# Kernel optimization log

Hardware: AMD Instinct MI355X
Metric: run time of the kernel (lower is better)

## Reference

```python
import jax, jax.numpy as jnp
import numpy as np

BETA = 0.25
ENTROPY_LOSS_RATIO = 0.1
TEMPERATURE = 0.01
EPS = 1e-5


def _l2norm(x):
    return x / jnp.sqrt(jnp.sum(x * x, axis=-1, keepdims=True)).clip(1e-12)


def _entropy_loss(affinity):
    # affinity: [N, n_e]
    a = affinity / TEMPERATURE
    probs = jax.nn.softmax(a, axis=-1)
    log_probs = jax.nn.log_softmax(a + EPS, axis=-1)
    avg_probs = jnp.mean(probs, axis=0)
    avg_entropy = -jnp.sum(avg_probs * jnp.log(avg_probs + EPS))
    sample_entropy = -jnp.mean(jnp.sum(probs * log_probs, axis=-1))
    return sample_entropy - avg_entropy


def setup_inputs() -> dict:
    key = jax.random.key(0)
    k1, k2, k3 = jax.random.split(key, 3)
    B, C, H, W = 16, 256, 32, 32
    n_e = 16384
    z = jax.random.normal(k1, (B, C, H, W), dtype=jnp.float32)
    embedding = jax.random.normal(k2, (n_e, C), dtype=jnp.float32) * 0.02
    query_ids = jax.random.randint(k3, (B, 1), 0, W, dtype=jnp.int64)
    return {"z": z, "embedding": embedding, "query_ids": query_ids}


def reference(z, embedding, query_ids):
    B, C, H, W = z.shape
    sg = jax.lax.stop_gradient
    zt = jnp.transpose(z, (0, 2, 3, 1))            # [B,H,W,C]
    # l2_norm=True path
    zt = _l2norm(zt)
    emb = _l2norm(embedding)                       # [n_e, C]
    zf = zt.reshape(-1, C)                         # [N, C]
    d = (jnp.sum(zf * zf, axis=1, keepdims=True)
         + jnp.sum(emb * emb, axis=1)
         - 2.0 * jnp.einsum('nd,kd->nk', zf, emb))  # [N, n_e]
    idx = jnp.argmin(d, axis=1)                    # [N]
    z_q = emb[idx].reshape(zt.shape)               # [B,H,W,C]

    # dead code rate (unbiased std over batch, per token position)
    code = idx.reshape(B, -1).astype(jnp.float32)
    dead_code_rate = jnp.mean((jnp.std(code, axis=0, ddof=1) < 1e-5).astype(jnp.float32))

    vq_loss = jnp.mean((z_q - sg(zt)) ** 2, axis=-1, keepdims=True)      # [B,H,W,1]
    commit_loss = BETA * jnp.mean((sg(z_q) - zt) ** 2, axis=-1, keepdims=True)
    loss_mask = (jnp.arange(W).reshape(1, 1, -1, 1)
                 <= query_ids[:, -1].reshape(-1, 1, 1, 1)).astype(jnp.float32)
    denom = jnp.sum(loss_mask)
    vq_loss = jnp.sum(vq_loss * loss_mask) / denom
    commit_loss = jnp.sum(commit_loss * loss_mask) / denom
    entropy_loss = ENTROPY_LOSS_RATIO * _entropy_loss(-d)

    # straight-through estimator
    z_q_st = zt + sg(z_q - zt)
    z_q_out = jnp.transpose(z_q_st, (0, 3, 1, 2))  # [B,C,H,W]
    return (z_q_out, vq_loss, commit_loss, entropy_loss, dead_code_rate, idx)
```

## Files before the change

kernel.cpp:

```cpp
#include <hip/hip_runtime.h>
#include <math.h>

#define N_TOK   16384
#define N_E     16384
#define CDIM    256
#define NCH     8
#define CHSZ    (N_E / NCH)
#define L2E100  144.26950408889634f
#define DELTA_C 0.06f
#define EPS_NT  0.008f
#define CAP_BLK 1536u
#define NT_CAP  65536u

typedef __attribute__((ext_vector_type(8))) short short8;
typedef __attribute__((ext_vector_type(4))) float f32x4;

#define OFF_A2   0u
#define OFF_B2   2097152u
#define OFF_RMX  4194304u
#define OFF_CS   4210688u
#define OFF_SC   4227072u
#define OFF_RK   4227088u
#define OFF_NT   4259856u
#define OFF_NTC  4325392u
#define OFF_CBC  4325408u
#define OFF_IDX  4327456u
#define OFF_CAND 4343840u
#define OFF_ZT   10635296u
#define NEED_ZT_BYTES 59318400ull

__device__ __forceinline__ unsigned short f2bf(float x) {
  unsigned u = __float_as_uint(x);
  unsigned r = (u + 0x7fffu + ((u >> 16) & 1u)) >> 16;
  return (unsigned short)r;
}
__device__ __forceinline__ float bf2f(unsigned short h) {
  return __uint_as_float(((unsigned)h) << 16);
}
__device__ __forceinline__ unsigned fkey(float f) {
  unsigned u = __float_as_uint(f);
  return (u & 0x80000000u) ? ~u : (u | 0x80000000u);
}
__device__ __forceinline__ float keyf(unsigned k) {
  return (k & 0x80000000u) ? __uint_as_float(k ^ 0x80000000u) : __uint_as_float(~k);
}

__device__ __forceinline__ void async_load16(const void* g, void* l) {
  __builtin_amdgcn_global_load_lds((const __attribute__((address_space(1))) void*)g,
                                   (__attribute__((address_space(3))) void*)l, 16, 0, 0);
}

__device__ __forceinline__ float blockReduceSum256(float v, float* sbuf) {
  __syncthreads();
  v += __shfl_down(v, 32);
  v += __shfl_down(v, 16);
  v += __shfl_down(v, 8);
  v += __shfl_down(v, 4);
  v += __shfl_down(v, 2);
  v += __shfl_down(v, 1);
  const int tid = threadIdx.x;
  if ((tid & 63) == 0) sbuf[tid >> 6] = v;
  __syncthreads();
  return sbuf[0] + sbuf[1] + sbuf[2] + sbuf[3];
}

__global__ __launch_bounds__(256) void k_norm_emb(const float* __restrict__ emb,
    unsigned short* __restrict__ B2, float* __restrict__ colsum,
    float* __restrict__ scalars, unsigned long long* __restrict__ rowkey,
    unsigned* __restrict__ ntc, unsigned* __restrict__ rowMaxU) {
  const int tid = threadIdx.x, lane = tid & 63, wv = tid >> 6;
  if (blockIdx.x < 64) {
    const int i = blockIdx.x * 256 + tid;
    colsum[i] = 0.f;
    rowkey[i] = ~0ull;
    rowMaxU[i] = 0u;
    if (i < 16) { scalars[i] = 0.f; ntc[i] = 0u; }
  }
  const int k = blockIdx.x * 4 + wv;
  const float4 v = *(const float4*)&emb[(size_t)k * CDIM + lane * 4];
  float ss = v.x * v.x + v.y * v.y + v.z * v.z + v.w * v.w;
#pragma unroll
  for (int off = 1; off < 64; off <<= 1) ss += __shfl_xor(ss, off);
  const float r = 1.0f / fmaxf(sqrtf(ss), 1e-12f);
  ushort4 o;
  o.x = f2bf(v.x * r); o.y = f2bf(v.y * r);
  o.z = f2bf(v.z * r); o.w = f2bf(v.w * r);
  *(ushort4*)&B2[(size_t)k * CDIM + lane * 4] = o;
}

__global__ __launch_bounds__(256) void k_norm_z(const float* __restrict__ z,
                                                unsigned short* __restrict__ A2,
                                                float* __restrict__ zT) {
  __shared__ float ssb[4][64];
  __shared__ float rn[64];
  __shared__ unsigned short tile[64 * 264];
  __shared__ float tileF[64 * 260];
  const int b = blockIdx.x >> 4, hw0 = (blockIdx.x & 15) * 64;
  const int tid = threadIdx.x, cg = tid >> 6, hwl = tid & 63;
  float ss = 0.f;
#pragma unroll 8
  for (int i = 0; i < 64; ++i) {
    const int c = cg + i * 4;
    const float x = z[((size_t)(b * CDIM + c) << 10) + hw0 + hwl];
    ss = fmaf(x, x, ss);
  }
  ssb[cg][hwl] = ss;
  __syncthreads();
  if (tid < 64) {
    const float t = ssb[0][tid] + ssb[1][tid] + ssb[2][tid] + ssb[3][tid];
    rn[tid] = 1.0f / fmaxf(sqrtf(t), 1e-12f);
  }
  __syncthreads();
  const float r = rn[hwl];
#pragma unroll 8
  for (int i = 0; i < 64; ++i) {
    const int c = cg + i * 4;
    const float x = z[((size_t)(b * CDIM + c) << 10) + hw0 + hwl];
    tile[hwl * 264 + c] = f2bf(x * r);
    tileF[hwl * 260 + c] = x;
  }
  __syncthreads();
  const int rr = tid >> 5, tt = tid & 31;
#pragma unroll
  for (int it = 0; it < 8; ++it) {
    const int row = rr + 8 * it;
    const int token = b * 1024 + hw0 + row;
    const uint4 v = *(const uint4*)&tile[row * 264 + tt * 8];
    *(uint4*)&A2[(size_t)token * CDIM + tt * 8] = v;
    if (zT != nullptr) {
      const float4 f0 = *(const float4*)&tileF[row * 260 + tt * 4];
      const float4 f1 = *(const float4*)&tileF[row * 260 + 128 + tt * 4];
      *(float4*)&zT[(size_t)token * CDIM + tt * 4] = f0;
      *(float4*)&zT[(size_t)token * CDIM + 128 + tt * 4] = f1;
    }
  }
}

__global__ __launch_bounds__(256, 3) void k_pass1(const unsigned short* __restrict__ A2,
    const unsigned short* __restrict__ B2,
    unsigned long long* __restrict__ cand, unsigned* __restrict__ cbc,
    unsigned* __restrict__ rowMaxU) {
  __shared__ alignas(16) unsigned short Bt[2][128 * 64];
  __shared__ unsigned smaxU[64];
  __shared__ unsigned lcnt;
  const int rt = blockIdx.x, chunk = blockIdx.y;
  const int r0 = rt * 64, k0 = chunk * CHSZ;
  const int blin = rt * NCH + chunk;
  const int tid = threadIdx.x, lane = tid & 63, w = tid >> 6;
  const int wrr = (w & 1) * 32, wc = (w >> 1) * 64;
  const int l15 = lane & 15, quad = lane >> 4;

  if (tid == 0) lcnt = 0u;
  if (tid < 64) smaxU[tid] = 0u;

  short8 afr[2][4][2];
#pragma unroll
  for (int ti = 0; ti < 2; ++ti) {
    const size_t rbase = (size_t)(r0 + wrr + ti * 16 + l15) * CDIM;
#pragma unroll
    for (int st = 0; st < 4; ++st)
#pragma unroll
      for (int kk = 0; kk < 2; ++kk)
        afr[ti][st][kk] = *(const short8*)&A2[rbase + st * 64 + (((kk << 2) | quad) * 8)];
  }

  const unsigned short* bsrc[4];
  unsigned bdst[4];
#pragma unroll
  for (int i = 0; i < 4; ++i) {
    const int lin = i * 256 + tid;
    const int row = lin >> 3, cg = lin & 7;
    const int gcg = cg ^ (row & 7);
    bsrc[i] = B2 + (size_t)(k0 + row) * CDIM + gcg * 8;
    bdst[i] = (unsigned)lin * 16u;
  }
#pragma unroll
  for (int i = 0; i < 4; ++i)
    async_load16(bsrc[i], (char*)Bt[0] + bdst[i]);

  int boff[4][2];
#pragma unroll
  for (int tj = 0; tj < 4; ++tj) {
    const int br = wc + tj * 16 + l15;
#pragma unroll
    for (int kk = 0; kk < 2; ++kk)
      boff[tj][kk] = br * 64 + ((((kk << 2) | quad) ^ (br & 7)) * 8);
  }
  __syncthreads();

  f32x4 acc[2][4];

  for (int ct = 0; ct < 16; ++ct) {
#pragma unroll
    for (int ti = 0; ti < 2; ++ti)
#pragma unroll
      for (int tj = 0; tj < 4; ++tj) acc[ti][tj] = (f32x4){0.f, 0.f, 0.f, 0.f};

#pragma unroll
    for (int st = 0; st < 4; ++st) {
      if (!(ct == 15 && st == 3)) {
        const int noff = (st < 3) ? (st + 1) * 64 : 32768;
        char* dbuf = (char*)Bt[(st + 1) & 1];
#pragma unroll
        for (int i = 0; i < 4; ++i)
          async_load16(bsrc[i] + noff, dbuf + bdst[i]);
      }
      const unsigned short* bp = Bt[st & 1];
#pragma unroll
      for (int kk = 0; kk < 2; ++kk) {
        short8 bfr[4];
#pragma unroll
        for (int tj = 0; tj < 4; ++tj)
          bfr[tj] = *(const short8*)&bp[boff[tj][kk]];
#pragma unroll
        for (int ti = 0; ti < 2; ++ti)
#pragma unroll
          for (int tj = 0; tj < 4; ++tj)
            acc[ti][tj] = __builtin_amdgcn_mfma_f32_16x16x32_bf16(afr[ti][st][kk], bfr[tj],
                                                                  acc[ti][tj], 0, 0, 0);
      }
      if (st == 3) {
        const int kb = k0 + ct * 128;
#pragma unroll
        for (int ti = 0; ti < 2; ++ti)
#pragma unroll
          for (int tj = 0; tj < 4; ++tj) {
            f32x4 a = acc[ti][tj];
#pragma unroll
            for (int r = 0; r < 4; ++r) a[r] = a[r] + a[r];
            acc[ti][tj] = a;
          }
#pragma unroll
        for (int ti = 0; ti < 2; ++ti)
#pragma unroll
          for (int r = 0; r < 4; ++r) {
            float mt = fmaxf(fmaxf(acc[ti][0][r], acc[ti][1][r]),
                             fmaxf(acc[ti][2][r], acc[ti][3][r]));
            mt = fmaxf(mt, __shfl_xor(mt, 1));
            mt = fmaxf(mt, __shfl_xor(mt, 2));
            mt = fmaxf(mt, __shfl_xor(mt, 4));
            mt = fmaxf(mt, __shfl_xor(mt, 8));
            if (l15 == 0) atomicMax(&smaxU[wrr + ti * 16 + quad * 4 + r], fkey(mt));
          }
        __syncthreads();
#pragma unroll
        for (int ti = 0; ti < 2; ++ti)
#pragma unroll
          for (int r = 0; r < 4; ++r) {
            const int rowloc = wrr + ti * 16 + quad * 4 + r;
            const float thr = keyf(smaxU[rowloc]) - DELTA_C;
            const unsigned rowg = (unsigned)(r0 + rowloc);
#pragma unroll
            for (int tj = 0; tj < 4; ++tj) {
              const float t = acc[ti][tj][r];
              if (t >= thr) {
                const unsigned slot = atomicAdd(&lcnt, 1u);
                if (slot < CAP_BLK) {
                  const unsigned pr = (rowg << 14) | (unsigned)(kb + wc + tj * 16 + l15);
                  cand[(size_t)blin * CAP_BLK + slot] =
                      ((unsigned long long)__float_as_uint(t) << 32) | pr;
                }
              }
            }
          }
      }
      __syncthreads();
    }
#pragma unroll
    for (int i = 0; i < 4; ++i) bsrc[i] += 32768;
  }
  if (tid < 64) atomicMax(&rowMaxU[r0 + tid], smaxU[tid]);
  if (tid == 0) cbc[blin] = lcnt < CAP_BLK ? lcnt : CAP_BLK;
}

__global__ __launch_bounds__(256) void k_cstat2(const unsigned long long* __restrict__ cand,
    const unsigned* __restrict__ cbc, const unsigned* __restrict__ rowMaxU,
    float* __restrict__ colsum, unsigned* __restrict__ ntList,
    unsigned* __restrict__ ntc, float* __restrict__ scalars) {
  __shared__ float lM[64], lZ[64], lE[64], lIZ[64];
  __shared__ float sbuf[4];
  const int rt = blockIdx.x, r0 = rt * 64;
  const int tid = threadIdx.x, lane = tid & 63;
  if (tid < 64) {
    lM[tid] = keyf(rowMaxU[r0 + tid]);
    lZ[tid] = 0.f; lE[tid] = 0.f;
  }
  __syncthreads();
  for (int sub = 0; sub < NCH; ++sub) {
    const int blin = rt * NCH + sub;
    const unsigned cnt = cbc[blin] < CAP_BLK ? cbc[blin] : CAP_BLK;
    for (unsigned i = tid; i < cnt; i += 256u) {
      const unsigned long long e = cand[(size_t)blin * CAP_BLK + i];
      const unsigned pr = (unsigned)(e & 0xFFFFFFFu);
      const float t = __uint_as_float((unsigned)(e >> 32));
      const int rowl = (int)((pr >> 14) & 63u);
      const float d = t - lM[rowl];
      const float ex = exp2f(d * L2E100);
      atomicAdd(&lZ[rowl], ex);
      atomicAdd(&lE[rowl], d * 100.0f * ex);
    }
  }
  __syncthreads();
  float ent = 0.f;
  if (tid < 64) {
    const float Z = lZ[tid];
    lIZ[tid] = 1.0f / Z;
    ent = logf(Z) - lE[tid] / Z;
  }
  const float es = blockReduceSum256(ent, sbuf);
  if (tid == 0) atomicAdd(&scalars[1], es);
  __syncthreads();
  for (int sub = 0; sub < NCH; ++sub) {
    const int blin = rt * NCH + sub;
    const unsigned cnt = cbc[blin] < CAP_BLK ? cbc[blin] : CAP_BLK;
    const unsigned lim = (cnt + 255u) & ~255u;
    for (unsigned i = tid; i < lim; i += 256u) {
      bool nt = false;
      unsigned pr = 0u;
      if (i < cnt) {
        const unsigned long long e = cand[(size_t)blin * CAP_BLK + i];
        pr = (unsigned)(e & 0xFFFFFFFu);
        const float t = __uint_as_float((unsigned)(e >> 32));
        const int rowl = (int)((pr >> 14) & 63u);
        const float d = t - lM[rowl];
        atomicAdd(&colsum[pr & 0x3FFFu], exp2f(d * L2E100) * lIZ[rowl]);
        nt = (d >= -EPS_NT);
      }
      const unsigned long long mask = __ballot(nt);
      const unsigned cw = (unsigned)__popcll(mask);
      unsigned base = 0u;
      if (lane == 0 && cw) base = atomicAdd(ntc, cw);
      base = __shfl((int)base, 0);
      if (nt) {
        const unsigned off = (unsigned)__popcll(mask & ((1ull << lane) - 1ull));
        const unsigned s = base + off;
        if (s < NT_CAP) ntList[s] = pr;
      }
    }
  }
}

__global__ __launch_bounds__(256) void k_refine(const float* __restrict__ z,
    const float* __restrict__ zT, const float* __restrict__ emb,
    const unsigned* __restrict__ ntList, const unsigned* __restrict__ ntc,
    unsigned long long* __restrict__ rowkey) {
  const unsigned cnt = *ntc;
  const unsigned lim = cnt < NT_CAP ? cnt : NT_CAP;
  const int lane = threadIdx.x & 63, wv = threadIdx.x >> 6;
  for (unsigned slot = blockIdx.x * 4 + wv; slot < lim; slot += gridDim.x * 4) {
    const unsigned pr = ntList[slot];
    const int n = (int)(pr >> 14), k = (int)(pr & 0x3FFFu);
    const int b = n >> 10, hw = n & 1023;
    double sz = 0.0, se = 0.0, sp = 0.0;
#pragma unroll
    for (int u = 0; u < CDIM / 64; ++u) {
      const int c = lane + u * 64;
      const double zv = (zT != nullptr)
          ? (double)zT[(size_t)n * CDIM + c]
          : (double)z[((size_t)(b * CDIM + c) << 10) + hw];
      const double ev = (double)emb[(size_t)k * CDIM + c];
      sz = fma(zv, zv, sz); se = fma(ev, ev, se); sp = fma(zv, ev, sp);
    }
    for (int off = 32; off; off >>= 1) {
      sz += __shfl_down(sz, off);
      se += __shfl_down(se, off);
      sp += __shfl_down(sp, off);
    }
    if (lane == 0) {
      const double nz = fmax(sqrt(sz), 1e-12);
      const double ne = fmax(sqrt(se), 1e-12);
      const double d = sz / (nz * nz) + se / (ne * ne) - 2.0 * sp / (nz * ne);
      const unsigned long long key =
          (((unsigned long long)(d * 140737488355328.0)) << 14) | (unsigned long long)k;
      atomicMin(&rowkey[n], key);
    }
  }
}

__global__ __launch_bounds__(256) void k_zq(const unsigned short* __restrict__ A2,
    const unsigned short* __restrict__ B2, const unsigned long long* __restrict__ rowkey,
    const long long* __restrict__ qids, int* __restrict__ idxI,
    float* __restrict__ outIdxF, float* __restrict__ outZ,
    float* __restrict__ scalars) {
  __shared__ int lidx[64];
  __shared__ unsigned short tile[64 * 264];
  __shared__ float sbuf[4];
  const int b = blockIdx.x >> 4, hw0 = (blockIdx.x & 15) * 64;
  const int tid = threadIdx.x;
  if (tid < 64) {
    const int n = b * 1024 + hw0 + tid;
    const unsigned long long key = rowkey[n];
    const int k = (key != ~0ull) ? (int)(key & 0x3FFFull) : 0;
    lidx[tid] = k;
    idxI[n] = k;
    outIdxF[n] = (float)k;
  }
  __syncthreads();
  const long long qid = qids[b];
  const int rr = tid >> 5, tt = tid & 31;
  float vq = 0.f;
#pragma unroll
  for (int it = 0; it < 8; ++it) {
    const int row = rr + 8 * it;
    const int token = b * 1024 + hw0 + row;
    union { uint4 v; unsigned short s[8]; } ev, zv;
    ev.v = *(const uint4*)&B2[(size_t)lidx[row] * CDIM + tt * 8];
    zv.v = *(const uint4*)&A2[(size_t)token * CDIM + tt * 8];
    *(uint4*)&tile[row * 264 + tt * 8] = ev.v;
    float dd = 0.f;
#pragma unroll
    for (int u = 0; u < 8; ++u) {
      const float d = bf2f(ev.s[u]) - bf2f(zv.s[u]);
      dd = fmaf(d, d, dd);
    }
    if ((long long)(row & 31) <= qid) vq += dd;
  }
  const float s = blockReduceSum256(vq, sbuf);
  if (tid == 0) atomicAdd(&scalars[0], s * (1.0f / 256.0f));
  __syncthreads();
  const int cg = tid >> 6, hwl = tid & 63;
#pragma unroll 8
  for (int i = 0; i < 64; ++i) {
    const int c = cg + i * 4;
    outZ[((size_t)(b * CDIM + c) << 10) + hw0 + hwl] = bf2f(tile[hwl * 264 + c]);
  }
}

__global__ __launch_bounds__(256) void k_final(const int* __restrict__ idxI,
    const long long* __restrict__ qids, const float* __restrict__ colsum,
    const float* __restrict__ scalars, float* __restrict__ out) {
  __shared__ float sbuf[4];
  const int tid = threadIdx.x;
  float ae = 0.f;
  for (int i = tid; i < N_E; i += 256) {
    const float q = colsum[i] * (1.0f / (float)N_TOK);
    ae += q * logf(q + 1e-5f);
  }
  const float aes = blockReduceSum256(ae, sbuf);
  int cnt = 0;
  for (int p = tid; p < 1024; p += 256) {
    const int v = idxI[p];
    bool eq = true;
    for (int b = 1; b < 16; ++b) eq = eq && (idxI[b * 1024 + p] == v);
    cnt += eq ? 1 : 0;
  }
  const float dc = blockReduceSum256((float)cnt, sbuf);
  if (tid == 0) {
    float denom = 0.f;
    for (int b = 0; b < 16; ++b) denom += (float)(qids[b] + 1ll);
    out[4194304] = scalars[0] / denom;
    out[4194305] = 0.25f * scalars[0] / denom;
    out[4194306] = 0.1f * (scalars[1] * (1.0f / (float)N_TOK) + aes);
    out[4194307] = dc * (1.0f / 1024.0f);
  }
}

extern "C" void kernel_launch(void* const* d_in, const int* in_sizes, int n_in,
                              void* d_out, int out_size, void* d_ws, size_t ws_size,
                              hipStream_t stream) {
  const float*      z    = (const float*)d_in[0];
  const float*      emb  = (const float*)d_in[1];
  const long long*  qids = (const long long*)d_in[2];
  float* out = (float*)d_out;
  float* W   = (float*)d_ws;

  unsigned short* A2 = (unsigned short*)(W + OFF_A2);
  unsigned short* B2 = (unsigned short*)(W + OFF_B2);
  unsigned* rowMaxU = (unsigned*)(W + OFF_RMX);
  float* colsum = W + OFF_CS;
  float* scal   = W + OFF_SC;
  unsigned long long* rowkey = (unsigned long long*)(W + OFF_RK);
  unsigned* ntList = (unsigned*)(W + OFF_NT);
  unsigned* ntc    = (unsigned*)(W + OFF_NTC);
  unsigned* cbc    = (unsigned*)(W + OFF_CBC);
  int* idxI        = (int*)(W + OFF_IDX);
  unsigned long long* cand = (unsigned long long*)(W + OFF_CAND);
  float* zT = (ws_size >= NEED_ZT_BYTES) ? (W + OFF_ZT) : (float*)nullptr;

  k_norm_emb<<<dim3(N_E / 4),     dim3(256), 0, stream>>>(emb, B2, colsum, scal,
                                                          rowkey, ntc, rowMaxU);
  k_norm_z  <<<dim3(256),         dim3(256), 0, stream>>>(z, A2, zT);
  k_pass1   <<<dim3(256, NCH),    dim3(256), 0, stream>>>(A2, B2, cand, cbc, rowMaxU);
  k_cstat2  <<<dim3(256),         dim3(256), 0, stream>>>(cand, cbc, rowMaxU, colsum,
                                                          ntList, ntc, scal);
  k_refine  <<<dim3(1024),        dim3(256), 0, stream>>>(z, zT, emb, ntList, ntc, rowkey);
  k_zq      <<<dim3(256),         dim3(256), 0, stream>>>(A2, B2, rowkey, qids,
                                                          idxI, out + 4194308, out, scal);
  k_final   <<<dim3(1),           dim3(256), 0, stream>>>(idxI, qids, colsum, scal, out);
}
```

Baseline: 641.3 us.

## Software-pipeline candidate epilogue behind next tile's MFMA with ping-pong accumulators

The GEMM-plus-candidate kernel now keeps two accumulator sets and runs the max-reduction and candidate-emit epilogue for the previous column tile while the MFMAs for the next tile are issued. The epilogue is split across the st==0 and st==1 stages, which also removes one extra __syncthreads per tile. MFMA sections are bracketed with s_setprio, and the per-lane B-load pointer arrays are replaced by a single base pointer plus constant offsets to save registers. In exchange, the doubled accumulators raise VGPR pressure, which could lower occupancy, and the last tile needs a duplicated epilogue after the loop.

```diff
diff --git a/kernel.cpp b/kernel.cpp
--- a/kernel.cpp
+++ b/kernel.cpp
@@ -164,19 +164,14 @@
         afr[ti][st][kk] = *(const short8*)&A2[rbase + st * 64 + (((kk << 2) | quad) * 8)];
   }
 
-  const unsigned short* bsrc[4];
-  unsigned bdst[4];
-#pragma unroll
-  for (int i = 0; i < 4; ++i) {
-    const int lin = i * 256 + tid;
-    const int row = lin >> 3, cg = lin & 7;
-    const int gcg = cg ^ (row & 7);
-    bsrc[i] = B2 + (size_t)(k0 + row) * CDIM + gcg * 8;
-    bdst[i] = (unsigned)lin * 16u;
-  }
+  const int row0 = tid >> 3, cg0 = tid & 7;
+  const int gcg0 = cg0 ^ (row0 & 7);
+  const unsigned short* bsrc0 = B2 + (size_t)(k0 + row0) * CDIM + gcg0 * 8;
+  const unsigned bofs0 = (unsigned)tid * 16u;
+
 #pragma unroll
   for (int i = 0; i < 4; ++i)
-    async_load16(bsrc[i], (char*)Bt[0] + bdst[i]);
+    async_load16(bsrc0 + i * 8192, (char*)Bt[0] + bofs0 + i * 4096);
 
   int boff[4][2];
 #pragma unroll
@@ -188,24 +183,28 @@
   }
   __syncthreads();
 
-  f32x4 acc[2][4];
-
-  for (int ct = 0; ct < 16; ++ct) {
+  f32x4 accA[2][4], accB[2][4];
+  size_t cbase = 0;
+
+  auto computeCt = [&](f32x4 (&aN)[2][4], f32x4 (&aO)[2][4], int ctNew, int doEpi) {
+    const int kbOld = k0 + (ctNew - 1) * 128;
+    const unsigned short* bs = bsrc0 + cbase;
 #pragma unroll
     for (int ti = 0; ti < 2; ++ti)
 #pragma unroll
-      for (int tj = 0; tj < 4; ++tj) acc[ti][tj] = (f32x4){0.f, 0.f, 0.f, 0.f};
+      for (int tj = 0; tj < 4; ++tj) aN[ti][tj] = (f32x4){0.f, 0.f, 0.f, 0.f};
 
 #pragma unroll
     for (int st = 0; st < 4; ++st) {
-      if (!(ct == 15 && st == 3)) {
+      if (!(ctNew == 15 && st == 3)) {
         const int noff = (st < 3) ? (st + 1) * 64 : 32768;
         char* dbuf = (char*)Bt[(st + 1) & 1];
 #pragma unroll
         for (int i = 0; i < 4; ++i)
-          async_load16(bsrc[i] + noff, dbuf + bdst[i]);
+          async_load16(bs + i * 8192 + noff, dbuf + bofs0 + i * 4096);
       }
       const unsigned short* bp = Bt[st & 1];
+      __builtin_amdgcn_s_setprio(1);
 #pragma unroll
       for (int kk = 0; kk < 2; ++kk) {
         short8 bfr[4];
@@ -216,33 +215,35 @@
         for (int ti = 0; ti < 2; ++ti)
 #pragma unroll
           for (int tj = 0; tj < 4; ++tj)
-            acc[ti][tj] = __builtin_amdgcn_mfma_f32_16x16x32_bf16(afr[ti][st][kk], bfr[tj],
-                                                                  acc[ti][tj], 0, 0, 0);
-      }
-      if (st == 3) {
-        const int kb = k0 + ct * 128;
+            aN[ti][tj] = __builtin_amdgcn_mfma_f32_16x16x32_bf16(afr[ti][st][kk], bfr[tj],
+                                                                 aN[ti][tj], 0, 0, 0);
+      }
+      __builtin_amdgcn_s_setprio(0);
+
+      if (doEpi && st == 0) {
 #pragma unroll
         for (int ti = 0; ti < 2; ++ti)
 #pragma unroll
           for (int tj = 0; tj < 4; ++tj) {
-            f32x4 a = acc[ti][tj];
+            f32x4 a = aO[ti][tj];
 #pragma unroll
             for (int r = 0; r < 4; ++r) a[r] = a[r] + a[r];
-            acc[ti][tj] = a;
+            aO[ti][tj] = a;
           }
 #pragma unroll
         for (int ti = 0; ti < 2; ++ti)
 #pragma unroll
           for (int r = 0; r < 4; ++r) {
-            float mt = fmaxf(fmaxf(acc[ti][0][r], acc[ti][1][r]),
-                             fmaxf(acc[ti][2][r], acc[ti][3][r]));
+            float mt = fmaxf(fmaxf(aO[ti][0][r], aO[ti][1][r]),
+                             fmaxf(aO[ti][2][r], aO[ti][3][r]));
             mt = fmaxf(mt, __shfl_xor(mt, 1));
             mt = fmaxf(mt, __shfl_xor(mt, 2));
             mt = fmaxf(mt, __shfl_xor(mt, 4));
             mt = fmaxf(mt, __shfl_xor(mt, 8));
             if (l15 == 0) atomicMax(&smaxU[wrr + ti * 16 + quad * 4 + r], fkey(mt));
           }
-        __syncthreads();
+      }
+      if (doEpi && st == 1) {
 #pragma unroll
         for (int ti = 0; ti < 2; ++ti)
 #pragma unroll
@@ -252,11 +253,11 @@
             const unsigned rowg = (unsigned)(r0 + rowloc);
 #pragma unroll
             for (int tj = 0; tj < 4; ++tj) {
-              const float t = acc[ti][tj][r];
+              const float t = aO[ti][tj][r];
               if (t >= thr) {
                 const unsigned slot = atomicAdd(&lcnt, 1u);
                 if (slot < CAP_BLK) {
-                  const unsigned pr = (rowg << 14) | (unsigned)(kb + wc + tj * 16 + l15);
+                  const unsigned pr = (rowg << 14) | (unsigned)(kbOld + wc + tj * 16 + l15);
                   cand[(size_t)blin * CAP_BLK + slot] =
                       ((unsigned long long)__float_as_uint(t) << 32) | pr;
                 }
@@ -266,9 +267,63 @@
       }
       __syncthreads();
     }
-#pragma unroll
-    for (int i = 0; i < 4; ++i) bsrc[i] += 32768;
-  }
+    cbase += 32768;
+  };
+
+  computeCt(accA, accB, 0, 0);
+#pragma unroll 1
+  for (int ctp = 0; ctp < 7; ++ctp) {
+    computeCt(accB, accA, 2 * ctp + 1, 1);
+    computeCt(accA, accB, 2 * ctp + 2, 1);
+  }
+  computeCt(accB, accA, 15, 1);
+
+  {
+    const int kb = k0 + 15 * 128;
+#pragma unroll
+    for (int ti = 0; ti < 2; ++ti)
+#pragma unroll
+      for (int tj = 0; tj < 4; ++tj) {
+        f32x4 a = accB[ti][tj];
+#pragma unroll
+        for (int r = 0; r < 4; ++r) a[r] = a[r] + a[r];
+        accB[ti][tj] = a;
+      }
+#pragma unroll
+    for (int ti = 0; ti < 2; ++ti)
+#pragma unroll
+      for (int r = 0; r < 4; ++r) {
+        float mt = fmaxf(fmaxf(accB[ti][0][r], accB[ti][1][r]),
+                         fmaxf(accB[ti][2][r], accB[ti][3][r]));
+        mt = fmaxf(mt, __shfl_xor(mt, 1));
+        mt = fmaxf(mt, __shfl_xor(mt, 2));
+        mt = fmaxf(mt, __shfl_xor(mt, 4));
+        mt = fmaxf(mt, __shfl_xor(mt, 8));
+        if (l15 == 0) atomicMax(&smaxU[wrr + ti * 16 + quad * 4 + r], fkey(mt));
+      }
+    __syncthreads();
+#pragma unroll
+    for (int ti = 0; ti < 2; ++ti)
+#pragma unroll
+      for (int r = 0; r < 4; ++r) {
+        const int rowloc = wrr + ti * 16 + quad * 4 + r;
+        const float thr = keyf(smaxU[rowloc]) - DELTA_C;
+        const unsigned rowg = (unsigned)(r0 + rowloc);
+#pragma unroll
+        for (int tj = 0; tj < 4; ++tj) {
+          const float t = accB[ti][tj][r];
+          if (t >= thr) {
+            const unsigned slot = atomicAdd(&lcnt, 1u);
+            if (slot < CAP_BLK) {
+              const unsigned pr = (rowg << 14) | (unsigned)(kb + wc + tj * 16 + l15);
+              cand[(size_t)blin * CAP_BLK + slot] =
+                  ((unsigned long long)__float_as_uint(t) << 32) | pr;
+            }
+          }
+        }
+      }
+  }
+  __syncthreads();
   if (tid < 64) atomicMax(&rowMaxU[r0 + tid], smaxU[tid]);
   if (tid == 0) cbc[blin] = lcnt < CAP_BLK ? lcnt : CAP_BLK;
 }
```

After: 960.1 us. 1.5x slower.

## Triple-buffer B tiles in pass1 with fine-grained vmcnt waits and priority hints

Applied to the files above, without the earlier changes.

The distance GEMM kernel moves from double to triple buffering of the codebook tile in LDS, so loads run two stages ahead. Full __syncthreads are replaced with explicit s_waitcnt vmcnt(4) plus raw s_barrier, letting one stage's loads stay in flight across the barrier. It also raises wave priority around the MFMA block. This hides global-load latency but uses more LDS per block, which may reduce occupancy, and relies on the hand-written waitcnt counts being correct.

```diff
diff --git a/kernel.cpp b/kernel.cpp
--- a/kernel.cpp
+++ b/kernel.cpp
@@ -140,7 +140,7 @@
     const unsigned short* __restrict__ B2,
     unsigned long long* __restrict__ cand, unsigned* __restrict__ cbc,
     unsigned* __restrict__ rowMaxU) {
-  __shared__ alignas(16) unsigned short Bt[2][128 * 64];
+  __shared__ alignas(16) unsigned short Bt[3][128 * 64];
   __shared__ unsigned smaxU[64];
   __shared__ unsigned lcnt;
   const int rt = blockIdx.x, chunk = blockIdx.y;
@@ -164,19 +164,10 @@
         afr[ti][st][kk] = *(const short8*)&A2[rbase + st * 64 + (((kk << 2) | quad) * 8)];
   }
 
-  const unsigned short* bsrc[4];
-  unsigned bdst[4];
-#pragma unroll
-  for (int i = 0; i < 4; ++i) {
-    const int lin = i * 256 + tid;
-    const int row = lin >> 3, cg = lin & 7;
-    const int gcg = cg ^ (row & 7);
-    bsrc[i] = B2 + (size_t)(k0 + row) * CDIM + gcg * 8;
-    bdst[i] = (unsigned)lin * 16u;
-  }
-#pragma unroll
-  for (int i = 0; i < 4; ++i)
-    async_load16(bsrc[i], (char*)Bt[0] + bdst[i]);
+  const int row0 = tid >> 3, cg0 = tid & 7;
+  const int gcg0 = cg0 ^ (row0 & 7);
+  const unsigned short* bsrc0 = B2 + (size_t)(k0 + row0) * CDIM + gcg0 * 8;
+  const unsigned bofs0 = (unsigned)tid * 16u;
 
   int boff[4][2];
 #pragma unroll
@@ -186,10 +177,25 @@
     for (int kk = 0; kk < 2; ++kk)
       boff[tj][kk] = br * 64 + ((((kk << 2) | quad) ^ (br & 7)) * 8);
   }
-  __syncthreads();
+
+#pragma unroll
+  for (int i = 0; i < 4; ++i)
+    async_load16(bsrc0 + i * 8192, (char*)Bt[0] + bofs0 + i * 4096);
+#pragma unroll
+  for (int i = 0; i < 4; ++i)
+    async_load16(bsrc0 + i * 8192 + 64, (char*)Bt[1] + bofs0 + i * 4096);
+  asm volatile("s_waitcnt vmcnt(4) lgkmcnt(0)" ::: "memory");
+  __builtin_amdgcn_s_barrier();
+  __builtin_amdgcn_sched_barrier(0);
+
+  unsigned short* bufR = Bt[0];
+  unsigned short* bufN = Bt[1];
+  unsigned short* bufW = Bt[2];
 
   f32x4 acc[2][4];
-
+  size_t cb = 0;
+
+#pragma unroll 1
   for (int ct = 0; ct < 16; ++ct) {
 #pragma unroll
     for (int ti = 0; ti < 2; ++ti)
@@ -198,20 +204,21 @@
 
 #pragma unroll
     for (int st = 0; st < 4; ++st) {
-      if (!(ct == 15 && st == 3)) {
-        const int noff = (st < 3) ? (st + 1) * 64 : 32768;
-        char* dbuf = (char*)Bt[(st + 1) & 1];
+      if (!(ct == 15 && st >= 2)) {
+        const size_t noff = cb + ((st < 2) ? (size_t)((st + 2) * 64)
+                                           : (size_t)(32768 + (st - 2) * 64));
 #pragma unroll
         for (int i = 0; i < 4; ++i)
-          async_load16(bsrc[i] + noff, dbuf + bdst[i]);
+          async_load16(bsrc0 + noff + i * 8192, (char*)bufW + bofs0 + i * 4096);
       }
-      const unsigned short* bp = Bt[st & 1];
+
+      __builtin_amdgcn_s_setprio(1);
 #pragma unroll
       for (int kk = 0; kk < 2; ++kk) {
         short8 bfr[4];
 #pragma unroll
         for (int tj = 0; tj < 4; ++tj)
-          bfr[tj] = *(const short8*)&bp[boff[tj][kk]];
+          bfr[tj] = *(const short8*)&bufR[boff[tj][kk]];
 #pragma unroll
         for (int ti = 0; ti < 2; ++ti)
 #pragma unroll
@@ -219,6 +226,8 @@
             acc[ti][tj] = __builtin_amdgcn_mfma_f32_16x16x32_bf16(afr[ti][st][kk], bfr[tj],
                                                                   acc[ti][tj], 0, 0, 0);
       }
+      __builtin_amdgcn_s_setprio(0);
+
       if (st == 3) {
         const int kb = k0 + ct * 128;
 #pragma unroll
@@ -242,7 +251,9 @@
             mt = fmaxf(mt, __shfl_xor(mt, 8));
             if (l15 == 0) atomicMax(&smaxU[wrr + ti * 16 + quad * 4 + r], fkey(mt));
           }
-        __syncthreads();
+        asm volatile("s_waitcnt lgkmcnt(0)" ::: "memory");
+        __builtin_amdgcn_s_barrier();
+        __builtin_amdgcn_sched_barrier(0);
 #pragma unroll
         for (int ti = 0; ti < 2; ++ti)
 #pragma unroll
@@ -264,11 +275,21 @@
             }
           }
       }
-      __syncthreads();
-    }
-#pragma unroll
-    for (int i = 0; i < 4; ++i) bsrc[i] += 32768;
-  }
+
+      {
+        unsigned short* tmp = bufR; bufR = bufN; bufN = bufW; bufW = tmp;
+      }
+      if (ct == 15 && st == 2)
+        asm volatile("s_waitcnt vmcnt(0)" ::: "memory");
+      else
+        asm volatile("s_waitcnt vmcnt(4)" ::: "memory");
+      __builtin_amdgcn_s_barrier();
+      __builtin_amdgcn_sched_barrier(0);
+    }
+    cb += 32768;
+  }
+
+  __syncthreads();
   if (tid < 64) atomicMax(&rowMaxU[r0 + tid], smaxU[tid]);
   if (tid == 0) cbc[blin] = lcnt < CAP_BLK ? lcnt : CAP_BLK;
 }
```

Result: slower. 654.8 us (+2.1%).

## Give each wave full row ownership in pass1 to drop shared max and barrier

Applied to the files above, without the earlier changes.

Changes the pass1 GEMM warp tiling from 2x2 waves (32 rows by 64 columns) to each wave owning 16 full rows across all 128 columns. Because a wave now sees a row's entire column tile, the row max is kept in registers, which removes the shared-memory atomicMax and the extra __syncthreads per column tile. Candidate filtering is done on the un-doubled dot product with a halved threshold, and the doubling is applied only to stored candidates. The trade-off is that A-fragment reuse drops (each B fragment serves one A tile instead of two), so more LDS reads are issued per MFMA.

```diff
diff --git a/kernel.cpp b/kernel.cpp
--- a/kernel.cpp
+++ b/kernel.cpp
@@ -8,6 +8,7 @@
 #define CHSZ    (N_E / NCH)
 #define L2E100  144.26950408889634f
 #define DELTA_C 0.06f
+#define DELTA_D 0.03f
 #define EPS_NT  0.008f
 #define CAP_BLK 1536u
 #define NT_CAP  65536u
@@ -141,60 +142,54 @@
     unsigned long long* __restrict__ cand, unsigned* __restrict__ cbc,
     unsigned* __restrict__ rowMaxU) {
   __shared__ alignas(16) unsigned short Bt[2][128 * 64];
-  __shared__ unsigned smaxU[64];
   __shared__ unsigned lcnt;
   const int rt = blockIdx.x, chunk = blockIdx.y;
   const int r0 = rt * 64, k0 = chunk * CHSZ;
   const int blin = rt * NCH + chunk;
   const int tid = threadIdx.x, lane = tid & 63, w = tid >> 6;
-  const int wrr = (w & 1) * 32, wc = (w >> 1) * 64;
+  const int wr0 = w * 16;
   const int l15 = lane & 15, quad = lane >> 4;
 
   if (tid == 0) lcnt = 0u;
-  if (tid < 64) smaxU[tid] = 0u;
-
-  short8 afr[2][4][2];
-#pragma unroll
-  for (int ti = 0; ti < 2; ++ti) {
-    const size_t rbase = (size_t)(r0 + wrr + ti * 16 + l15) * CDIM;
+
+  short8 afr[4][2];
+  {
+    const size_t rbase = (size_t)(r0 + wr0 + l15) * CDIM;
 #pragma unroll
     for (int st = 0; st < 4; ++st)
 #pragma unroll
       for (int kk = 0; kk < 2; ++kk)
-        afr[ti][st][kk] = *(const short8*)&A2[rbase + st * 64 + (((kk << 2) | quad) * 8)];
-  }
-
-  const unsigned short* bsrc[4];
-  unsigned bdst[4];
-#pragma unroll
-  for (int i = 0; i < 4; ++i) {
-    const int lin = i * 256 + tid;
-    const int row = lin >> 3, cg = lin & 7;
-    const int gcg = cg ^ (row & 7);
-    bsrc[i] = B2 + (size_t)(k0 + row) * CDIM + gcg * 8;
-    bdst[i] = (unsigned)lin * 16u;
-  }
-#pragma unroll
-  for (int i = 0; i < 4; ++i)
-    async_load16(bsrc[i], (char*)Bt[0] + bdst[i]);
-
-  int boff[4][2];
-#pragma unroll
-  for (int tj = 0; tj < 4; ++tj) {
-    const int br = wc + tj * 16 + l15;
+        afr[st][kk] = *(const short8*)&A2[rbase + st * 64 + (((kk << 2) | quad) * 8)];
+  }
+
+  const int row0 = tid >> 3, cg0 = tid & 7;
+  const int gcg0 = cg0 ^ (row0 & 7);
+  const unsigned short* bsrc0 = B2 + (size_t)(k0 + row0) * CDIM + gcg0 * 8;
+  const unsigned bofs0 = (unsigned)tid * 16u;
+
+  int boff[8][2];
+#pragma unroll
+  for (int tj = 0; tj < 8; ++tj) {
+    const int br = tj * 16 + l15;
 #pragma unroll
     for (int kk = 0; kk < 2; ++kk)
       boff[tj][kk] = br * 64 + ((((kk << 2) | quad) ^ (br & 7)) * 8);
   }
-  __syncthreads();
-
-  f32x4 acc[2][4];
-
+
+#pragma unroll
+  for (int i = 0; i < 4; ++i)
+    async_load16(bsrc0 + i * 8192, (char*)Bt[0] + bofs0 + i * 4096);
+  __syncthreads();
+
+  f32x4 acc[8];
+  float runMax[4];
+#pragma unroll
+  for (int r = 0; r < 4; ++r) runMax[r] = -3.0e38f;
+
+#pragma unroll 1
   for (int ct = 0; ct < 16; ++ct) {
 #pragma unroll
-    for (int ti = 0; ti < 2; ++ti)
-#pragma unroll
-      for (int tj = 0; tj < 4; ++tj) acc[ti][tj] = (f32x4){0.f, 0.f, 0.f, 0.f};
+    for (int tj = 0; tj < 8; ++tj) acc[tj] = (f32x4){0.f, 0.f, 0.f, 0.f};
 
 #pragma unroll
     for (int st = 0; st < 4; ++st) {
@@ -203,73 +198,59 @@
         char* dbuf = (char*)Bt[(st + 1) & 1];
 #pragma unroll
         for (int i = 0; i < 4; ++i)
-          async_load16(bsrc[i] + noff, dbuf + bdst[i]);
+          async_load16(bsrc0 + noff + i * 8192, dbuf + bofs0 + i * 4096);
       }
       const unsigned short* bp = Bt[st & 1];
 #pragma unroll
       for (int kk = 0; kk < 2; ++kk) {
-        short8 bfr[4];
-#pragma unroll
-        for (int tj = 0; tj < 4; ++tj)
+        short8 bfr[8];
+#pragma unroll
+        for (int tj = 0; tj < 8; ++tj)
           bfr[tj] = *(const short8*)&bp[boff[tj][kk]];
 #pragma unroll
-        for (int ti = 0; ti < 2; ++ti)
-#pragma unroll
-          for (int tj = 0; tj < 4; ++tj)
-            acc[ti][tj] = __builtin_amdgcn_mfma_f32_16x16x32_bf16(afr[ti][st][kk], bfr[tj],
-                                                                  acc[ti][tj], 0, 0, 0);
+        for (int tj = 0; tj < 8; ++tj)
+          acc[tj] = __builtin_amdgcn_mfma_f32_16x16x32_bf16(afr[st][kk], bfr[tj],
+                                                            acc[tj], 0, 0, 0);
       }
+
       if (st == 3) {
         const int kb = k0 + ct * 128;
 #pragma unroll
-        for (int ti = 0; ti < 2; ++ti)
-#pragma unroll
-          for (int tj = 0; tj < 4; ++tj) {
-            f32x4 a = acc[ti][tj];
-#pragma unroll
-            for (int r = 0; r < 4; ++r) a[r] = a[r] + a[r];
-            acc[ti][tj] = a;
-          }
-#pragma unroll
-        for (int ti = 0; ti < 2; ++ti)
-#pragma unroll
-          for (int r = 0; r < 4; ++r) {
-            float mt = fmaxf(fmaxf(acc[ti][0][r], acc[ti][1][r]),
-                             fmaxf(acc[ti][2][r], acc[ti][3][r]));
-            mt = fmaxf(mt, __shfl_xor(mt, 1));
-            mt = fmaxf(mt, __shfl_xor(mt, 2));
-            mt = fmaxf(mt, __shfl_xor(mt, 4));
-            mt = fmaxf(mt, __shfl_xor(mt, 8));
-            if (l15 == 0) atomicMax(&smaxU[wrr + ti * 16 + quad * 4 + r], fkey(mt));
-          }
-        __syncthreads();
-#pragma unroll
-        for (int ti = 0; ti < 2; ++ti)
-#pragma unroll
-          for (int r = 0; r < 4; ++r) {
-            const int rowloc = wrr + ti * 16 + quad * 4 + r;
-            const float thr = keyf(smaxU[rowloc]) - DELTA_C;
-            const unsigned rowg = (unsigned)(r0 + rowloc);
-#pragma unroll
-            for (int tj = 0; tj < 4; ++tj) {
-              const float t = acc[ti][tj][r];
-              if (t >= thr) {
-                const unsigned slot = atomicAdd(&lcnt, 1u);
-                if (slot < CAP_BLK) {
-                  const unsigned pr = (rowg << 14) | (unsigned)(kb + wc + tj * 16 + l15);
-                  cand[(size_t)blin * CAP_BLK + slot] =
-                      ((unsigned long long)__float_as_uint(t) << 32) | pr;
-                }
+        for (int r = 0; r < 4; ++r) {
+          float mt = acc[0][r];
+#pragma unroll
+          for (int tj = 1; tj < 8; ++tj) mt = fmaxf(mt, acc[tj][r]);
+          mt = fmaxf(mt, __shfl_xor(mt, 1));
+          mt = fmaxf(mt, __shfl_xor(mt, 2));
+          mt = fmaxf(mt, __shfl_xor(mt, 4));
+          mt = fmaxf(mt, __shfl_xor(mt, 8));
+          runMax[r] = fmaxf(runMax[r], mt);
+          const float thrD = runMax[r] - DELTA_D;
+          const unsigned rowg = (unsigned)(r0 + wr0 + quad * 4 + r);
+#pragma unroll
+          for (int tj = 0; tj < 8; ++tj) {
+            const float d = acc[tj][r];
+            if (d >= thrD) {
+              const unsigned slot = atomicAdd(&lcnt, 1u);
+              if (slot < CAP_BLK) {
+                const float t = d + d;
+                const unsigned pr = (rowg << 14) | (unsigned)(kb + tj * 16 + l15);
+                cand[(size_t)blin * CAP_BLK + slot] =
+                    ((unsigned long long)__float_as_uint(t) << 32) | pr;
               }
             }
           }
+        }
       }
       __syncthreads();
     }
-#pragma unroll
-    for (int i = 0; i < 4; ++i) bsrc[i] += 32768;
-  }
-  if (tid < 64) atomicMax(&rowMaxU[r0 + tid], smaxU[tid]);
+    bsrc0 += 32768;
+  }
+
+#pragma unroll
+  for (int r = 0; r < 4; ++r)
+    if (l15 == 0)
+      atomicMax(&rowMaxU[r0 + wr0 + quad * 4 + r], fkey(runMax[r] + runMax[r]));
   if (tid == 0) cbc[blin] = lcnt < CAP_BLK ? lcnt : CAP_BLK;
 }
 
```

After: 548.5 us. 14.5% less time.
